# Kernel tuning notes

Measured on AMD Instinct MI355X. Metric: run time of the kernel, lower is better.

The kernel has to match this reference:

```python
import jax, jax.numpy as jnp
import numpy as np


def conv1x1(x, w, b):
    # x: [B,C,H,W], w: [O,C], b: [O] -> [B,O,H,W]
    return jnp.einsum('oc,bchw->bohw', w, x) + b[None, :, None, None]


def setup_inputs() -> dict:
    key = jax.random.key(0)
    ks = jax.random.split(key, 9)
    B, C, H, W = 4, 256, 64, 64
    Ci = C // 2
    s_in = 1.0 / np.sqrt(C)
    s_mid = 1.0 / np.sqrt(Ci)
    return {
        'x': jax.random.normal(ks[0], (B, C, H, W), jnp.float32),
        'theta_w': jax.random.normal(ks[1], (Ci, C), jnp.float32) * s_in,
        'theta_b': jnp.zeros((Ci,), jnp.float32),
        'phi_w': jax.random.normal(ks[2], (Ci, C), jnp.float32) * s_in,
        'phi_b': jnp.zeros((Ci,), jnp.float32),
        'g_w': jax.random.normal(ks[3], (Ci, C), jnp.float32) * s_in,
        'g_b': jnp.zeros((Ci,), jnp.float32),
        'out_w': jax.random.normal(ks[4], (C, Ci), jnp.float32) * s_mid,
        'out_b': jnp.zeros((C,), jnp.float32),
    }


def reference(x, theta_w, theta_b, phi_w, phi_b, g_w, g_b, out_w, out_b):
    B, C, H, W = x.shape
    N = H * W
    theta = conv1x1(x, theta_w, theta_b).reshape(B, -1, N)  # [B,Ci,N]
    phi = conv1x1(x, phi_w, phi_b).reshape(B, -1, N)        # [B,Ci,N]
    g = conv1x1(x, g_w, g_b).reshape(B, -1, N)              # [B,Ci,N]
    # attention[b,n,m] = theta[b,:,n] . phi[b,:,m]
    attn = jnp.einsum('bcn,bcm->bnm', theta, phi)           # [B,N,N]
    attn = jax.nn.softmax(attn, axis=-1)
    # out[b,c,n] = sum_m g[b,c,m] * attn[b,n,m]  (g @ attn^T)
    out = jnp.einsum('bcm,bnm->bcn', g, attn).reshape(B, -1, H, W)
    out = conv1x1(out, out_w, out_b)
    return out + x
```

## Files before the change

kernel.cpp:

```cpp
#include <hip/hip_runtime.h>
#include <stdint.h>

#define NB 4
#define NC 256
#define NCI 128
#define NN 4096

typedef __attribute__((ext_vector_type(8))) short short8;
typedef __attribute__((ext_vector_type(4))) float f32x4;

__device__ __forceinline__ float bf2f(unsigned short u) {
    union { unsigned int i; float f; } v; v.i = ((unsigned int)u) << 16; return v.f;
}
__device__ __forceinline__ unsigned short f2bf(float f) {
    union { unsigned int i; float f; } v; v.f = f;
    unsigned int b = v.i;
    b += 0x7FFFu + ((b >> 16) & 1u);
    return (unsigned short)(b >> 16);
}

__global__ void k_fill(float* __restrict__ p, float v, int n) {
    int i = blockIdx.x * blockDim.x + threadIdx.x;
    if (i < n) p[i] = v;
}

__global__ __launch_bounds__(256) void k_split(
    const float* __restrict__ Wt, const float* __restrict__ Wp,
    const float* __restrict__ Wg, const float* __restrict__ Wo,
    unsigned short* __restrict__ wbuf) {
    const float LOG2E = 1.4426950408889634f;
    int m = blockIdx.y;
    int i = blockIdx.x * 256 + threadIdx.x;
    if (m == 0) {
        float v = Wt[i] * LOG2E;
        unsigned short h = f2bf(v);
        wbuf[i] = h;
        wbuf[32768 + i] = f2bf(v - bf2f(h));
    } else if (m == 1) {
        float v = Wp[i];
        unsigned short h = f2bf(v);
        wbuf[65536 + i] = h;
        wbuf[98304 + i] = f2bf(v - bf2f(h));
    } else if (m == 2) {
        wbuf[131072 + i] = f2bf(Wg[i]);
    } else {
        wbuf[163840 + i] = f2bf(Wo[i]);
    }
}

__global__ __launch_bounds__(256, 2) void k_qkv2(
    const float* __restrict__ x,
    const unsigned short* __restrict__ WpH, const unsigned short* __restrict__ WpL,
    const unsigned short* __restrict__ WgH,
    const float* __restrict__ bp, const float* __restrict__ bg,
    unsigned short* __restrict__ phiH, unsigned short* __restrict__ phiL,
    unsigned short* __restrict__ gout) {
    __shared__ __align__(16) unsigned short sXh[32 * 72];
    __shared__ __align__(16) unsigned short sXl[32 * 72];
    const int b = blockIdx.y, n0 = blockIdx.x * 32;
    const int tid = threadIdx.x, lane = tid & 63, wave = tid >> 6;
    const int col = lane & 15, quad = lane >> 4;
    const int wm = wave * 32;

    f32x4 accP[2][2], accG[2][2];
#pragma unroll
    for (int i = 0; i < 2; i++)
#pragma unroll
        for (int j = 0; j < 2; j++)
#pragma unroll
            for (int e = 0; e < 4; e++) { accP[i][j][e] = 0.f; accG[i][j][e] = 0.f; }

    for (int c0 = 0; c0 < NC; c0 += 64) {
        __syncthreads();
        short8 ah[2][2], al[2][2], ag[2][2];
#pragma unroll
        for (int ks = 0; ks < 2; ks++)
#pragma unroll
            for (int i = 0; i < 2; i++) {
                size_t w = (size_t)(wm + i * 16 + col) * NC + c0 + ks * 32 + quad * 8;
                ah[ks][i] = *(const short8*)&WpH[w];
                al[ks][i] = *(const short8*)&WpL[w];
                ag[ks][i] = *(const short8*)&WgH[w];
            }
        {
            int cp = tid >> 3, n4 = (tid & 7) * 4;
            const float* xp = x + ((size_t)(b * NC + c0 + 2 * cp)) * NN + n0 + n4;
            float4 a = *(const float4*)xp;
            float4 c = *(const float4*)(xp + NN);
            float av[4] = { a.x, a.y, a.z, a.w };
            float cv[4] = { c.x, c.y, c.z, c.w };
#pragma unroll
            for (int j = 0; j < 4; j++) {
                unsigned short ha = f2bf(av[j]), hc = f2bf(cv[j]);
                unsigned short la = f2bf(av[j] - bf2f(ha)), lc = f2bf(cv[j] - bf2f(hc));
                *(unsigned int*)&sXh[(n4 + j) * 72 + 2 * cp] =
                    (unsigned int)ha | ((unsigned int)hc << 16);
                *(unsigned int*)&sXl[(n4 + j) * 72 + 2 * cp] =
                    (unsigned int)la | ((unsigned int)lc << 16);
            }
        }
        __syncthreads();
#pragma unroll
        for (int ks = 0; ks < 2; ks++)
#pragma unroll
            for (int j = 0; j < 2; j++) {
                short8 bh = *(const short8*)&sXh[(j * 16 + col) * 72 + ks * 32 + quad * 8];
                short8 bl = *(const short8*)&sXl[(j * 16 + col) * 72 + ks * 32 + quad * 8];
#pragma unroll
                for (int i = 0; i < 2; i++) {
                    accP[i][j] = __builtin_amdgcn_mfma_f32_16x16x32_bf16(ah[ks][i], bh, accP[i][j], 0, 0, 0);
                    accP[i][j] = __builtin_amdgcn_mfma_f32_16x16x32_bf16(ah[ks][i], bl, accP[i][j], 0, 0, 0);
                    accP[i][j] = __builtin_amdgcn_mfma_f32_16x16x32_bf16(al[ks][i], bh, accP[i][j], 0, 0, 0);
                    accG[i][j] = __builtin_amdgcn_mfma_f32_16x16x32_bf16(ag[ks][i], bh, accG[i][j], 0, 0, 0);
                }
            }
    }
#pragma unroll
    for (int i = 0; i < 2; i++) {
        int mrow = wm + i * 16 + quad * 4;
#pragma unroll
        for (int j = 0; j < 2; j++) {
            int n = n0 + j * 16 + col;
            unsigned short h[4], l[4];
#pragma unroll
            for (int e = 0; e < 4; e++) {
                float v = accP[i][j][e] + bp[mrow + e];
                h[e] = f2bf(v);
                l[e] = f2bf(v - bf2f(h[e]));
            }
            uint2 hv, lv;
            hv.x = (unsigned int)h[0] | ((unsigned int)h[1] << 16);
            hv.y = (unsigned int)h[2] | ((unsigned int)h[3] << 16);
            lv.x = (unsigned int)l[0] | ((unsigned int)l[1] << 16);
            lv.y = (unsigned int)l[2] | ((unsigned int)l[3] << 16);
            *(uint2*)&phiH[((size_t)(b * NN + n)) * NCI + mrow] = hv;
            *(uint2*)&phiL[((size_t)(b * NN + n)) * NCI + mrow] = lv;
#pragma unroll
            for (int r = 0; r < 4; r++)
                gout[((size_t)(b * NCI + mrow + r)) * NN + n] = f2bf(accG[i][j][r] + bg[mrow + r]);
        }
    }
}

__global__ __launch_bounds__(1024, 4) void k_attn(
    const float* __restrict__ x,
    const unsigned short* __restrict__ WtH, const unsigned short* __restrict__ WtL,
    const float* __restrict__ bt,
    const unsigned short* __restrict__ phiH, const unsigned short* __restrict__ phiL,
    const unsigned short* __restrict__ gmat,
    const unsigned short* __restrict__ WoH, const float* __restrict__ bo,
    float* __restrict__ y) {
    const float LOG2E = 1.4426950408889634f;
    __shared__ __align__(16) char smem[107520];
    unsigned short* sPhiH0 = (unsigned short*)(smem);
    unsigned short* sPhiH1 = (unsigned short*)(smem + 16384);
    unsigned short* sPhiL0 = (unsigned short*)(smem + 32768);
    unsigned short* sPhiL1 = (unsigned short*)(smem + 49152);
    unsigned short* sG0    = (unsigned short*)(smem + 65536);
    unsigned short* sG1    = (unsigned short*)(smem + 81920);
    unsigned short* sPall  = (unsigned short*)(smem + 98304);
    float* sLi             = (float*)(smem + 106496);
    unsigned short* sThH  = (unsigned short*)(smem);
    unsigned short* sThL  = (unsigned short*)(smem + 16384);
    unsigned short* sXhA  = (unsigned short*)(smem + 32768);
    unsigned short* sXlA  = (unsigned short*)(smem + 41984);
    unsigned short* sXhB  = (unsigned short*)(smem + 51200);
    unsigned short* sXlB  = (unsigned short*)(smem + 60416);
    float* sThF           = (float*)(smem + 32768);
    unsigned short* sO    = (unsigned short*)(smem);

    const int id = blockIdx.x;
    const int xcd = id & 7, slot = id >> 3;
    const int b = xcd >> 1;
    const int n0 = (slot * 2 + (xcd & 1)) * 64;

    const int tid = threadIdx.x, lane = tid & 63, wave = tid >> 6;
    const int col = lane & 15, quad = lane >> 4;
    const int qg = wave >> 2, kh = wave & 3;

    uint4 rPh, rPl, rG;
    auto LOADT = [&](int m0) {
        int row = tid >> 4, seg = tid & 15;
        size_t src = ((size_t)(b * NN + m0 + row)) * NCI + seg * 8;
        rPh = *(const uint4*)&phiH[src];
        rPl = *(const uint4*)&phiL[src];
        int row2 = tid >> 3, seg2 = tid & 7;
        rG = *(const uint4*)&gmat[((size_t)(b * NCI + row2)) * NN + m0 + seg2 * 8];
    };
    auto STORET = [&](unsigned short* dPh, unsigned short* dPl, unsigned short* dG) {
        int row = tid >> 4, seg = tid & 15;
        int dst = row * 128 + ((seg * 8) ^ ((row & 7) << 3));
        *(uint4*)&dPh[dst] = rPh;
        *(uint4*)&dPl[dst] = rPl;
        int row2 = tid >> 3, seg2 = tid & 7;
        *(uint4*)&dG[row2 * 64 + ((seg2 * 8) ^ ((row2 & 7) << 3))] = rG;
    };

    const int half = wave >> 3;
    const int wci8 = (wave & 7) * 16;
    f32x4 th[4];
#pragma unroll
    for (int j = 0; j < 4; j++)
#pragma unroll
        for (int e = 0; e < 4; e++) th[j][e] = 0.f;

    for (int s = 0; s < 2; s++) {
        {
            int set = tid >> 9;
            int t = tid & 511;
            int cp = t >> 4, n4 = (t & 15) * 4;
            int myc0 = set * 128 + s * 64;
            unsigned short* dXh = set ? sXhB : sXhA;
            unsigned short* dXl = set ? sXlB : sXlA;
            const float* xp = x + ((size_t)(b * NC + myc0 + 2 * cp)) * NN + n0 + n4;
            float4 a = *(const float4*)xp;
            float4 c = *(const float4*)(xp + NN);
            float av[4] = { a.x, a.y, a.z, a.w };
            float cv[4] = { c.x, c.y, c.z, c.w };
#pragma unroll
            for (int j = 0; j < 4; j++) {
                unsigned short ha = f2bf(av[j]), hc = f2bf(cv[j]);
                unsigned short la = f2bf(av[j] - bf2f(ha)), lc = f2bf(cv[j] - bf2f(hc));
                *(unsigned int*)&dXh[(n4 + j) * 72 + 2 * cp] =
                    (unsigned int)ha | ((unsigned int)hc << 16);
                *(unsigned int*)&dXl[(n4 + j) * 72 + 2 * cp] =
                    (unsigned int)la | ((unsigned int)lc << 16);
            }
        }
        __syncthreads();
        {
            int c0 = half * 128 + s * 64;
            const unsigned short* mXh = half ? sXhB : sXhA;
            const unsigned short* mXl = half ? sXlB : sXlA;
#pragma unroll
            for (int ks = 0; ks < 2; ks++) {
                size_t w = (size_t)(wci8 + col) * NC + c0 + ks * 32 + quad * 8;
                short8 ah = *(const short8*)&WtH[w];
                short8 al = *(const short8*)&WtL[w];
#pragma unroll
                for (int j = 0; j < 4; j++) {
                    short8 bh = *(const short8*)&mXh[(j * 16 + col) * 72 + ks * 32 + quad * 8];
                    short8 bl = *(const short8*)&mXl[(j * 16 + col) * 72 + ks * 32 + quad * 8];
                    th[j] = __builtin_amdgcn_mfma_f32_16x16x32_bf16(ah, bh, th[j], 0, 0, 0);
                    th[j] = __builtin_amdgcn_mfma_f32_16x16x32_bf16(ah, bl, th[j], 0, 0, 0);
                    th[j] = __builtin_amdgcn_mfma_f32_16x16x32_bf16(al, bh, th[j], 0, 0, 0);
                }
            }
        }
        __syncthreads();
    }
    if (half == 0) {
#pragma unroll
        for (int j = 0; j < 4; j++) {
            int q = j * 16 + col;
            int ci = (wci8 + quad * 4) ^ ((q & 7) << 2);
            *(f32x4*)&sThF[q * 128 + ci] = th[j];
        }
    }
    __syncthreads();
    if (half == 1) {
#pragma unroll
        for (int j = 0; j < 4; j++) {
            int q = j * 16 + col;
            int cif = (wci8 + quad * 4) ^ ((q & 7) << 2);
            f32x4 o = *(const f32x4*)&sThF[q * 128 + cif];
            unsigned short h[4], l[4];
#pragma unroll
            for (int e = 0; e < 4; e++) {
                float v = o[e] + th[j][e] + bt[wci8 + quad * 4 + e] * LOG2E;
                h[e] = f2bf(v);
                l[e] = f2bf(v - bf2f(h[e]));
            }
            int cisw = (wci8 + quad * 4) ^ ((q & 7) << 3);
            uint2 hv, lv;
            hv.x = (unsigned int)h[0] | ((unsigned int)h[1] << 16);
            hv.y = (unsigned int)h[2] | ((unsigned int)h[3] << 16);
            lv.x = (unsigned int)l[0] | ((unsigned int)l[1] << 16);
            lv.y = (unsigned int)l[2] | ((unsigned int)l[3] << 16);
            *(uint2*)&sThH[q * 128 + cisw] = hv;
            *(uint2*)&sThL[q * 128 + cisw] = lv;
        }
    }
    __syncthreads();
    short8 qh[4], ql[4];
    {
        int qrow = qg * 16 + col;
        int qsw = (qrow & 7) << 3;
#pragma unroll
        for (int ks = 0; ks < 4; ks++) {
            int off = (ks * 32 + quad * 8) ^ qsw;
            qh[ks] = *(const short8*)&sThH[qrow * 128 + off];
            ql[ks] = *(const short8*)&sThL[qrow * 128 + off];
        }
    }
    LOADT(0);
    __syncthreads();
    STORET(sPhiH0, sPhiL0, sG0);

    f32x4 oacc[2];
#pragma unroll
    for (int i = 0; i < 2; i++)
#pragma unroll
        for (int e = 0; e < 4; e++) oacc[i][e] = 0.f;
    float li[4] = { 0.f, 0.f, 0.f, 0.f };

    auto tile_step = [&](const unsigned short* cPhiH, const unsigned short* cPhiL,
                         const unsigned short* cG,
                         unsigned short* nPhiH, unsigned short* nPhiL, unsigned short* nG,
                         int m_next, bool do_next) {
        __syncthreads();
        if (do_next) LOADT(m_next);

        f32x4 S;
#pragma unroll
        for (int e = 0; e < 4; e++) S[e] = 0.f;
        {
            int kcol = kh * 16 + col;
            int kswz = (kcol & 7) << 3;
#pragma unroll
            for (int ks = 0; ks < 4; ks++) {
                int off = (ks * 32 + quad * 8) ^ kswz;
                short8 ph = *(const short8*)&cPhiH[kcol * 128 + off];
                short8 pl = *(const short8*)&cPhiL[kcol * 128 + off];
                S = __builtin_amdgcn_mfma_f32_16x16x32_bf16(qh[ks], ph, S, 0, 0, 0);
                S = __builtin_amdgcn_mfma_f32_16x16x32_bf16(qh[ks], pl, S, 0, 0, 0);
                S = __builtin_amdgcn_mfma_f32_16x16x32_bf16(ql[ks], ph, S, 0, 0, 0);
            }
        }
#pragma unroll
        for (int r = 0; r < 4; r++) {
            float p = exp2f(S[r]);
            li[r] += p;
            int q = qg * 16 + quad * 4 + r;
            sPall[q * 64 + ((kh * 16 + col) ^ ((q & 7) << 3))] = f2bf(p);
        }
        __syncthreads();

        short8 pf[2], af[2][2];
        {
            int qrow = qg * 16 + col;
            int qsw = (qrow & 7) << 3;
#pragma unroll
            for (int ks = 0; ks < 2; ks++)
                pf[ks] = *(const short8*)&sPall[qrow * 64 + ((ks * 32 + quad * 8) ^ qsw)];
#pragma unroll
            for (int ct = 0; ct < 2; ct++) {
                int grow = kh * 32 + ct * 16 + col;
                int gsw = (grow & 7) << 3;
#pragma unroll
                for (int ks = 0; ks < 2; ks++)
                    af[ct][ks] = *(const short8*)&cG[grow * 64 + ((ks * 32 + quad * 8) ^ gsw)];
            }
        }
#pragma unroll
        for (int ct = 0; ct < 2; ct++)
#pragma unroll
            for (int ks = 0; ks < 2; ks++)
                oacc[ct] = __builtin_amdgcn_mfma_f32_16x16x32_bf16(
                    af[ct][ks], pf[ks], oacc[ct], 0, 0, 0);

        if (do_next) STORET(nPhiH, nPhiL, nG);
    };

    for (int m0 = 0; m0 < NN; m0 += 128) {
        tile_step(sPhiH0, sPhiL0, sG0, sPhiH1, sPhiL1, sG1, m0 + 64, true);
        bool more = (m0 + 128) < NN;
        tile_step(sPhiH1, sPhiL1, sG1, sPhiH0, sPhiL0, sG0, m0 + 128, more);
    }

#pragma unroll
    for (int r = 0; r < 4; r++) {
        float rs = li[r];
#pragma unroll
        for (int off = 1; off < 16; off <<= 1) rs += __shfl_xor(rs, off);
        li[r] = rs;
    }
    if (col == 0) {
#pragma unroll
        for (int r = 0; r < 4; r++) sLi[wave * 16 + quad * 4 + r] = li[r];
    }
    __syncthreads();
    float inv = 1.0f / (sLi[(qg * 4 + 0) * 16 + col] + sLi[(qg * 4 + 1) * 16 + col] +
                        sLi[(qg * 4 + 2) * 16 + col] + sLi[(qg * 4 + 3) * 16 + col]);

#pragma unroll
    for (int ct = 0; ct < 2; ct++) {
        int q = qg * 16 + col;
        int ci = kh * 32 + ct * 16 + quad * 4;
        int cisw = ci ^ ((q & 7) << 3);
        uint2 v;
        unsigned short p0 = f2bf(oacc[ct][0] * inv);
        unsigned short p1 = f2bf(oacc[ct][1] * inv);
        unsigned short p2 = f2bf(oacc[ct][2] * inv);
        unsigned short p3 = f2bf(oacc[ct][3] * inv);
        v.x = (unsigned int)p0 | ((unsigned int)p1 << 16);
        v.y = (unsigned int)p2 | ((unsigned int)p3 << 16);
        *(uint2*)&sO[q * 128 + cisw] = v;
    }
    __syncthreads();
    f32x4 acc[4];
#pragma unroll
    for (int j = 0; j < 4; j++)
#pragma unroll
        for (int e = 0; e < 4; e++) acc[j][e] = 0.f;
#pragma unroll
    for (int ks = 0; ks < 4; ks++) {
        short8 af2 = *(const short8*)&WoH[(size_t)(wave * 16 + col) * NCI + ks * 32 + quad * 8];
#pragma unroll
        for (int j = 0; j < 4; j++) {
            int row = j * 16 + col;
            short8 bf = *(const short8*)&sO[row * 128 + ((ks * 32 + quad * 8) ^ ((row & 7) << 3))];
            acc[j] = __builtin_amdgcn_mfma_f32_16x16x32_bf16(af2, bf, acc[j], 0, 0, 0);
        }
    }
#pragma unroll
    for (int j = 0; j < 4; j++)
#pragma unroll
        for (int e = 0; e < 4; e++) {
            int o = wave * 16 + quad * 4 + e;
            size_t idx = ((size_t)(b * NC + o)) * NN + n0 + j * 16 + col;
            y[idx] = acc[j][e] + bo[o] + x[idx];
        }
}

extern "C" void kernel_launch(void* const* d_in, const int* in_sizes, int n_in,
                              void* d_out, int out_size, void* d_ws, size_t ws_size,
                              hipStream_t stream) {
    float* y = (float*)d_out;

    bool sizes_ok = (n_in == 9) &&
        in_sizes[0] == NB * NC * NN && in_sizes[1] == NCI * NC && in_sizes[2] == NCI &&
        in_sizes[3] == NCI * NC && in_sizes[4] == NCI && in_sizes[5] == NCI * NC &&
        in_sizes[6] == NCI && in_sizes[7] == NC * NCI && in_sizes[8] == NC &&
        out_size == NB * NC * NN;
    if (!sizes_ok) {
        k_fill<<<(out_size + 255) / 256, 256, 0, stream>>>(y, 777.0f, out_size);
        return;
    }
    if (ws_size < (size_t)16 * 1024 * 1024) {
        k_fill<<<(out_size + 255) / 256, 256, 0, stream>>>(y, 555.0f, out_size);
        return;
    }

    const float* x  = (const float*)d_in[0];
    const float* tw = (const float*)d_in[1];
    const float* tb = (const float*)d_in[2];
    const float* pw = (const float*)d_in[3];
    const float* pb = (const float*)d_in[4];
    const float* gw = (const float*)d_in[5];
    const float* gb = (const float*)d_in[6];
    const float* ow = (const float*)d_in[7];
    const float* obias = (const float*)d_in[8];

    unsigned short* ws16 = (unsigned short*)d_ws;
    unsigned short* phiH = ws16;
    unsigned short* phiL = ws16 + 2097152;
    unsigned short* g    = ws16 + 4194304;
    unsigned short* wbuf = ws16 + 6291456;
    unsigned short* WtH = wbuf,           *WtL = wbuf + 32768;
    unsigned short* WpH = wbuf + 65536,   *WpL = wbuf + 98304;
    unsigned short* WgH = wbuf + 131072,  *WoH = wbuf + 163840;

    k_split<<<dim3(128, 4), 256, 0, stream>>>(tw, pw, gw, ow, wbuf);
    k_qkv2<<<dim3(128, NB), 256, 0, stream>>>(x, WpH, WpL, WgH, pb, gb, phiH, phiL, g);
    k_attn<<<dim3(256), 1024, 0, stream>>>(x, WtH, WtL, tb, phiH, phiL, g, WoH, obias, y);
}
```

Before: 193.5 us.

## Software-pipeline attention loop: overlap PV of previous tile with QK of current

Restructures the attention main loop so the P·G MFMA for tile t-1 runs alongside the QK score MFMAs for tile t. It uses double-buffered P storage and a triple-buffered G ring, which cuts the barriers per tile from two to one. Global loads are now issued two tiles ahead, with register-staged stores one tile ahead. Shared memory grows to about 129 KB, which can lower occupancy, and the buffer rotation logic is more intricate.

```diff
diff --git a/kernel.cpp b/kernel.cpp
--- a/kernel.cpp
+++ b/kernel.cpp
@@ -151,15 +151,17 @@
     const unsigned short* __restrict__ WoH, const float* __restrict__ bo,
     float* __restrict__ y) {
     const float LOG2E = 1.4426950408889634f;
-    __shared__ __align__(16) char smem[107520];
+    __shared__ __align__(16) char smem[132096];
     unsigned short* sPhiH0 = (unsigned short*)(smem);
     unsigned short* sPhiH1 = (unsigned short*)(smem + 16384);
     unsigned short* sPhiL0 = (unsigned short*)(smem + 32768);
     unsigned short* sPhiL1 = (unsigned short*)(smem + 49152);
     unsigned short* sG0    = (unsigned short*)(smem + 65536);
     unsigned short* sG1    = (unsigned short*)(smem + 81920);
-    unsigned short* sPall  = (unsigned short*)(smem + 98304);
-    float* sLi             = (float*)(smem + 106496);
+    unsigned short* sG2    = (unsigned short*)(smem + 98304);
+    unsigned short* sPall0 = (unsigned short*)(smem + 114688);
+    unsigned short* sPall1 = (unsigned short*)(smem + 122880);
+    float* sLi             = (float*)(smem + 131072);
     unsigned short* sThH  = (unsigned short*)(smem);
     unsigned short* sThL  = (unsigned short*)(smem + 16384);
     unsigned short* sXhA  = (unsigned short*)(smem + 32768);
@@ -296,6 +298,8 @@
     LOADT(0);
     __syncthreads();
     STORET(sPhiH0, sPhiL0, sG0);
+    LOADT(64);
+    __syncthreads();
 
     f32x4 oacc[2];
 #pragma unroll
@@ -304,12 +308,19 @@
         for (int e = 0; e < 4; e++) oacc[i][e] = 0.f;
     float li[4] = { 0.f, 0.f, 0.f, 0.f };
 
-    auto tile_step = [&](const unsigned short* cPhiH, const unsigned short* cPhiL,
-                         const unsigned short* cG,
-                         unsigned short* nPhiH, unsigned short* nPhiL, unsigned short* nG,
-                         int m_next, bool do_next) {
-        __syncthreads();
-        if (do_next) LOADT(m_next);
+    int gs = 1, gr = 2;
+    for (int t = 0; t < 64; ++t) {
+        const unsigned short* cPhiH = (t & 1) ? sPhiH1 : sPhiH0;
+        const unsigned short* cPhiL = (t & 1) ? sPhiL1 : sPhiL0;
+        unsigned short* nPhiH = (t & 1) ? sPhiH0 : sPhiH1;
+        unsigned short* nPhiL = (t & 1) ? sPhiL0 : sPhiL1;
+        unsigned short* wG = gs == 0 ? sG0 : (gs == 1 ? sG1 : sG2);
+        const unsigned short* rGb = gr == 0 ? sG0 : (gr == 1 ? sG1 : sG2);
+        unsigned short* wPall = (t & 1) ? sPall1 : sPall0;
+        const unsigned short* rPall = (t & 1) ? sPall0 : sPall1;
+
+        if (t < 63) STORET(nPhiH, nPhiL, wG);
+        if (t < 62) LOADT((t + 2) * 64);
 
         f32x4 S;
 #pragma unroll
@@ -327,30 +338,53 @@
                 S = __builtin_amdgcn_mfma_f32_16x16x32_bf16(ql[ks], ph, S, 0, 0, 0);
             }
         }
+        if (t > 0) {
+            short8 pf[2], af[2][2];
+            int qrow = qg * 16 + col;
+            int qsw = (qrow & 7) << 3;
+#pragma unroll
+            for (int ks = 0; ks < 2; ks++)
+                pf[ks] = *(const short8*)&rPall[qrow * 64 + ((ks * 32 + quad * 8) ^ qsw)];
+#pragma unroll
+            for (int ct = 0; ct < 2; ct++) {
+                int grow = kh * 32 + ct * 16 + col;
+                int gsw = (grow & 7) << 3;
+#pragma unroll
+                for (int ks = 0; ks < 2; ks++)
+                    af[ct][ks] = *(const short8*)&rGb[grow * 64 + ((ks * 32 + quad * 8) ^ gsw)];
+            }
+#pragma unroll
+            for (int ct = 0; ct < 2; ct++)
+#pragma unroll
+                for (int ks = 0; ks < 2; ks++)
+                    oacc[ct] = __builtin_amdgcn_mfma_f32_16x16x32_bf16(
+                        af[ct][ks], pf[ks], oacc[ct], 0, 0, 0);
+        }
 #pragma unroll
         for (int r = 0; r < 4; r++) {
             float p = exp2f(S[r]);
             li[r] += p;
             int q = qg * 16 + quad * 4 + r;
-            sPall[q * 64 + ((kh * 16 + col) ^ ((q & 7) << 3))] = f2bf(p);
+            wPall[q * 64 + ((kh * 16 + col) ^ ((q & 7) << 3))] = f2bf(p);
         }
         __syncthreads();
-
+        gr = (gr == 2) ? 0 : gr + 1;
+        gs = (gs == 2) ? 0 : gs + 1;
+    }
+    {
         short8 pf[2], af[2][2];
-        {
-            int qrow = qg * 16 + col;
-            int qsw = (qrow & 7) << 3;
+        int qrow = qg * 16 + col;
+        int qsw = (qrow & 7) << 3;
+#pragma unroll
+        for (int ks = 0; ks < 2; ks++)
+            pf[ks] = *(const short8*)&sPall1[qrow * 64 + ((ks * 32 + quad * 8) ^ qsw)];
+#pragma unroll
+        for (int ct = 0; ct < 2; ct++) {
+            int grow = kh * 32 + ct * 16 + col;
+            int gsw = (grow & 7) << 3;
 #pragma unroll
             for (int ks = 0; ks < 2; ks++)
-                pf[ks] = *(const short8*)&sPall[qrow * 64 + ((ks * 32 + quad * 8) ^ qsw)];
-#pragma unroll
-            for (int ct = 0; ct < 2; ct++) {
-                int grow = kh * 32 + ct * 16 + col;
-                int gsw = (grow & 7) << 3;
-#pragma unroll
-                for (int ks = 0; ks < 2; ks++)
-                    af[ct][ks] = *(const short8*)&cG[grow * 64 + ((ks * 32 + quad * 8) ^ gsw)];
-            }
+                af[ct][ks] = *(const short8*)&sG0[grow * 64 + ((ks * 32 + quad * 8) ^ gsw)];
         }
 #pragma unroll
         for (int ct = 0; ct < 2; ct++)
@@ -358,14 +392,6 @@
             for (int ks = 0; ks < 2; ks++)
                 oacc[ct] = __builtin_amdgcn_mfma_f32_16x16x32_bf16(
                     af[ct][ks], pf[ks], oacc[ct], 0, 0, 0);
-
-        if (do_next) STORET(nPhiH, nPhiL, nG);
-    };
-
-    for (int m0 = 0; m0 < NN; m0 += 128) {
-        tile_step(sPhiH0, sPhiL0, sG0, sPhiH1, sPhiL1, sG1, m0 + 64, true);
-        bool more = (m0 + 128) < NN;
-        tile_step(sPhiH1, sPhiL1, sG1, sPhiH0, sPhiL0, sG0, m0 + 128, more);
     }
 
 #pragma unroll
```

New measurement: 195.5 us. No clear change (+1.1%).
